# Kernel tuning notes

Hardware: AMD Instinct MI355X
Metric: run time of the kernel (lower is better)

The kernel has to match this reference:

```python
import jax, jax.numpy as jnp
import numpy as np

H = 16  # headNum
D = 1024  # d_model
DK = D // H


def setup_inputs() -> dict:
    key = jax.random.key(0)
    ks = jax.random.split(key, 11)
    B, S = 2, 2048
    scale = 1.0 / np.sqrt(D)
    inp = {
        'query': jax.random.normal(ks[0], (B, S, D), jnp.float32),
        'key':   jax.random.normal(ks[1], (B, S, D), jnp.float32),
        'value': jax.random.normal(ks[2], (B, S, D), jnp.float32),
        # nn.Linear params: W is [out, in], y = x @ W.T + b
        'Wq': jax.random.normal(ks[3], (D, D), jnp.float32) * scale,
        'bq': jnp.zeros((D,), jnp.float32),
        'Wk': jax.random.normal(ks[4], (D, D), jnp.float32) * scale,
        'bk': jnp.zeros((D,), jnp.float32),
        'Wv': jax.random.normal(ks[5], (D, D), jnp.float32) * scale,
        'bv': jnp.zeros((D,), jnp.float32),
        'Wo': jax.random.normal(ks[6], (D, D), jnp.float32) * scale,
        'bo': jnp.zeros((D,), jnp.float32),
    }
    return inp


def reference(query, key, value, Wq, bq, Wk, bk, Wv, bv, Wo, bo):
    B, S, _ = query.shape
    # projections (torch Linear: x @ W.T + b), split heads -> [B, H, S, DK]
    q = (query @ Wq.T + bq).reshape(B, S, H, DK).transpose(0, 2, 1, 3)
    k = (key   @ Wk.T + bk).reshape(B, S, H, DK).transpose(0, 2, 1, 3)
    v = (value @ Wv.T + bv).reshape(B, S, H, DK).transpose(0, 2, 1, 3)
    # scores [B, H, S, S] = Q K^T / sqrt(d_k)  (fully materialized, as in source)
    scores = jnp.einsum('bhqd,bhkd->bhqk', q, k) * (DK ** -0.5)
    p_attn = jax.nn.softmax(scores, axis=-1)  # dropout = identity (eval)
    x = jnp.einsum('bhqk,bhkd->bhqd', p_attn, v)
    x = x.transpose(0, 2, 1, 3).reshape(B, S, H * DK)
    return x @ Wo.T + bo
```

## Files before the change

### kernel.cpp

```cpp
#include <hip/hip_runtime.h>

#define BATCH 2
#define SEQ   2048
#define NH    16
#define DK    64
#define DM    1024
#define MROWS 4096
#define NX    4194304
#define NW    1048576

typedef __attribute__((ext_vector_type(8))) short bf16x8;
typedef __attribute__((ext_vector_type(4))) short bf16x4;
typedef __attribute__((ext_vector_type(4))) float f32x4;
typedef __attribute__((ext_vector_type(4))) unsigned short us16x4;
typedef __attribute__((ext_vector_type(2))) unsigned int u32x2;

#if __has_builtin(__builtin_amdgcn_mfma_f32_16x16x16bf16_1k)
#define MFMA16(a, b, c) __builtin_amdgcn_mfma_f32_16x16x16bf16_1k(a, b, c, 0, 0, 0)
#else
#define MFMA16(a, b, c) (c)
#endif

__device__ __forceinline__ unsigned short f2bf(float f) {
  unsigned int u = __builtin_bit_cast(unsigned int, f);
  u += 0x7FFFu + ((u >> 16) & 1u);
  return (unsigned short)(u >> 16);
}

__device__ __forceinline__ unsigned int pkbf(float hi, float lo) {
#if __has_builtin(__builtin_amdgcn_perm)
  return __builtin_amdgcn_perm(__builtin_bit_cast(unsigned int, hi),
                               __builtin_bit_cast(unsigned int, lo), 0x07060302u);
#else
  return (__builtin_bit_cast(unsigned int, hi) & 0xffff0000u) |
         (__builtin_bit_cast(unsigned int, lo) >> 16);
#endif
}

__device__ __forceinline__ void g2l16(void* lds, const void* g) {
  __builtin_amdgcn_global_load_lds(
      (const __attribute__((address_space(1))) void*)g,
      (__attribute__((address_space(3))) void*)lds, 16, 0, 0);
}

__global__ __launch_bounds__(256) void cast_all(
    const float* __restrict__ q, const float* __restrict__ k, const float* __restrict__ v,
    const float* __restrict__ wq, const float* __restrict__ wk,
    const float* __restrict__ wv, const float* __restrict__ wo,
    unsigned short* __restrict__ dst) {
  size_t e = ((size_t)blockIdx.x * 256 + threadIdx.x) * 4;
  const float* src;
  if      (e < (size_t)NX)        src = q  + e;
  else if (e < (size_t)2*NX)      src = k  + (e - (size_t)NX);
  else if (e < (size_t)3*NX)      src = v  + (e - (size_t)2*NX);
  else if (e < (size_t)3*NX+NW)   src = wq + (e - (size_t)3*NX);
  else if (e < (size_t)3*NX+2*NW) src = wk + (e - (size_t)3*NX-NW);
  else if (e < (size_t)3*NX+3*NW) src = wv + (e - (size_t)3*NX-2*NW);
  else                            src = wo + (e - (size_t)3*NX-3*NW);
  float4 f = *(const float4*)src;
  us16x4 o;
  o[0] = f2bf(f.x); o[1] = f2bf(f.y); o[2] = f2bf(f.z); o[3] = f2bf(f.w);
  *(us16x4*)(dst + e) = o;
}

template <int MODE, int BM>
__global__ __launch_bounds__(256) void gemm_bt(
    const unsigned short* __restrict__ Xbase, const unsigned short* __restrict__ Wbase,
    const float* __restrict__ b0, const float* __restrict__ b1, const float* __restrict__ b2,
    unsigned short* __restrict__ qkv_dst, float* __restrict__ fout, float qscale) {
  constexpr int IM = BM / 32;
  constexpr int ASHOTS = (BM * 32) / 2048;
  const int tid  = threadIdx.x;
  const int lane = tid & 63;
  const int w    = tid >> 6;
  const int wm   = w >> 1, wn = w & 1;
  const int x15  = lane & 15, quad = lane >> 4;
  const int row0 = blockIdx.x * BM;
  const int col0 = blockIdx.y * 128;
  const int z    = blockIdx.z;

  const unsigned short* A  = Xbase + (size_t)z * NX;
  const unsigned short* Wp = Wbase + (size_t)z * NW;
  const float* bias = (MODE == 0) ? (z == 0 ? b0 : (z == 1 ? b1 : b2)) : b0;
  const float zs = (MODE == 0 && z == 0) ? qscale : 1.0f;

  __shared__ __align__(16) unsigned short At[2][BM * 32];
  __shared__ __align__(16) unsigned short Bt[2][128 * 32];

  f32x4 acc[IM][4] = {};

  auto stage = [&](int buf, int kt) {
#pragma unroll
    for (int j = 0; j < ASHOTS; ++j) {
      int e = (j * 256 + tid) * 8;
      int r = e >> 5, c = e & 31;
      g2l16(&At[buf][e], A + (size_t)(row0 + r) * DM + kt + c);
    }
#pragma unroll
    for (int j = 0; j < 2; ++j) {
      int e = (j * 256 + tid) * 8;
      int r = e >> 5, c = e & 31;
      g2l16(&Bt[buf][e], Wp + (size_t)(col0 + r) * DM + kt + c);
    }
  };

  stage(0, 0);
  for (int it = 0; it < DM / 32; ++it) {
    const int cur = it & 1;
    __syncthreads();
    if (it + 1 < DM / 32) stage(cur ^ 1, (it + 1) * 32);
    bf16x8 af[IM], bfv[4];
#pragma unroll
    for (int i = 0; i < IM; ++i)
      af[i] = *(const bf16x8*)&At[cur][(wm * (BM / 2) + i * 16 + x15) * 32 + quad * 8];
#pragma unroll
    for (int jn = 0; jn < 4; ++jn)
      bfv[jn] = *(const bf16x8*)&Bt[cur][(wn * 64 + jn * 16 + x15) * 32 + quad * 8];
#pragma unroll
    for (int i = 0; i < IM; ++i)
#pragma unroll
      for (int jn = 0; jn < 4; ++jn)
        acc[i][jn] = __builtin_amdgcn_mfma_f32_16x16x32_bf16(af[i], bfv[jn], acc[i][jn], 0, 0, 0);
  }

#pragma unroll
  for (int jn = 0; jn < 4; ++jn) {
    const int n = col0 + wn * 64 + jn * 16 + x15;
    const float bv = bias[n];
#pragma unroll
    for (int i = 0; i < IM; ++i) {
      const int m0 = row0 + wm * (BM / 2) + i * 16 + quad * 4;
      if (MODE == 0 && z == 2) {
        us16x4 pk;
#pragma unroll
        for (int r = 0; r < 4; ++r) pk[r] = f2bf(acc[i][jn][r] + bv);
        const int b = m0 >> 11, s = m0 & 2047;
        const int h = n >> 6,  dk = n & 63;
        *(us16x4*)&qkv_dst[(size_t)2 * NX + (((size_t)(b * NH + h) * DK + dk) << 11) + s] = pk;
      } else {
#pragma unroll
        for (int r = 0; r < 4; ++r) {
          const int m = m0 + r;
          float val = (acc[i][jn][r] + bv) * zs;
          if (MODE == 0) {
            const int b = m >> 11, s = m & 2047;
            const int h = n >> 6,  dk = n & 63;
            qkv_dst[(size_t)z * NX + (((size_t)(b * NH + h) * SEQ + s) << 6) + dk] = f2bf(val);
          } else {
            fout[(size_t)m * DM + n] = val;
          }
        }
      }
    }
  }
}

__global__ __launch_bounds__(256, 2) void attn(
    const unsigned short* __restrict__ Qb, const unsigned short* __restrict__ Kb,
    const unsigned short* __restrict__ VTb, unsigned short* __restrict__ AO) {
  const int tid  = threadIdx.x;
  const int lane = tid & 63;
  const int w    = tid >> 6;
  const int x15  = lane & 15, quad = lane >> 4;
  const int lin = (int)(blockIdx.x | (blockIdx.y << 4) | (blockIdx.z << 8));
  const int swz = ((lin & 7) << 6) | (lin >> 3);
  const int qt = swz & 15;
  const int h  = (swz >> 4) & 15;
  const int b  = swz >> 8;
  const size_t bh = ((size_t)(b * NH + h)) * SEQ * DK;
  const unsigned short* Q  = Qb  + bh;
  const unsigned short* K  = Kb  + bh;
  const unsigned short* VT = VTb + bh;
  const int q0 = qt * 128 + w * 32;

  __shared__ __align__(16) unsigned short Kl[2][64 * 64];
  __shared__ __align__(16) unsigned short Vl[2][64 * 64];

  bf16x8 qf[2][2];
#pragma unroll
  for (int qg = 0; qg < 2; ++qg)
#pragma unroll
    for (int ks = 0; ks < 2; ++ks)
      qf[qg][ks] = *(const bf16x8*)&Q[(size_t)(q0 + qg * 16 + x15) * DK + ks * 32 + quad * 8];

  f32x4 po[2][4] = {};
  f32x4 pol[2] = {};
  const bf16x4 vone = {(short)0x3F80, (short)0x3F80, (short)0x3F80, (short)0x3F80};

  const int sK0 = tid >> 3,          sK1 = (tid + 256) >> 3;
  const int dgK0 = (tid & 7) ^ (sK0 & 7), dgK1 = (tid & 7) ^ (sK1 & 7);

  auto stageKV = [&](int buf, int s0) {
    g2l16(&Kl[buf][(size_t)tid * 8],         K + (size_t)(s0 + sK0) * DK + dgK0 * 8);
    g2l16(&Kl[buf][(size_t)(tid + 256) * 8], K + (size_t)(s0 + sK1) * DK + dgK1 * 8);
    g2l16(&Vl[buf][(size_t)tid * 8],         VT + (size_t)sK0 * SEQ + s0 + dgK0 * 8);
    g2l16(&Vl[buf][(size_t)(tid + 256) * 8], VT + (size_t)sK1 * SEQ + s0 + dgK1 * 8);
  };

  stageKV(0, 0);
  for (int s0 = 0; s0 < SEQ; s0 += 64) {
    const int cur = (s0 >> 6) & 1;
    __syncthreads();
    if (s0 + 64 < SEQ) stageKV(cur ^ 1, s0 + 64);

    bf16x8 kf[4][2];
#pragma unroll
    for (int sh = 0; sh < 4; ++sh) {
      const int kbase = (sh * 16 + x15) * 8;
      kf[sh][0] = *(const bf16x8*)&Kl[cur][(kbase + ((0 + quad) ^ (x15 & 7))) * 8];
      kf[sh][1] = *(const bf16x8*)&Kl[cur][(kbase + ((4 + quad) ^ (x15 & 7))) * 8];
    }
    bf16x4 vf[4][4];
#pragma unroll
    for (int sh = 0; sh < 4; ++sh)
#pragma unroll
      for (int nt = 0; nt < 4; ++nt) {
        const int d = nt * 16 + x15;
        const int sg = (sh * 2 + (quad >> 1)) ^ (d & 7);
        vf[sh][nt] = *(const bf16x4*)&Vl[cur][(d * 8 + sg) * 8 + (quad & 1) * 4];
      }

#pragma unroll
    for (int sh = 0; sh < 4; ++sh) {
      bf16x4 pf[2];
#pragma unroll
      for (int qg = 0; qg < 2; ++qg) {
        f32x4 sacc = {};
        sacc = __builtin_amdgcn_mfma_f32_16x16x32_bf16(kf[sh][0], qf[qg][0], sacc, 0, 0, 0);
        sacc = __builtin_amdgcn_mfma_f32_16x16x32_bf16(kf[sh][1], qf[qg][1], sacc, 0, 0, 0);
        float p0 = __builtin_amdgcn_exp2f(sacc[0]);
        float p1 = __builtin_amdgcn_exp2f(sacc[1]);
        float p2 = __builtin_amdgcn_exp2f(sacc[2]);
        float p3 = __builtin_amdgcn_exp2f(sacc[3]);
        u32x2 uu;
        uu[0] = pkbf(p1, p0);
        uu[1] = pkbf(p3, p2);
        pf[qg] = __builtin_bit_cast(bf16x4, uu);
        pol[qg] = MFMA16(vone, pf[qg], pol[qg]);
      }

#pragma unroll
      for (int nt = 0; nt < 4; ++nt) {
        po[0][nt] = MFMA16(vf[sh][nt], pf[0], po[0][nt]);
        po[1][nt] = MFMA16(vf[sh][nt], pf[1], po[1][nt]);
      }
    }
  }

#pragma unroll
  for (int qg = 0; qg < 2; ++qg) {
    const float inv = 1.0f / pol[qg][0];
    const int s = q0 + qg * 16 + x15;
#pragma unroll
    for (int nt = 0; nt < 4; ++nt) {
      us16x4 pk;
#pragma unroll
      for (int r = 0; r < 4; ++r) pk[r] = f2bf(po[qg][nt][r] * inv);
      const int d = nt * 16 + quad * 4;
      *(us16x4*)&AO[((size_t)(b * SEQ + s)) * DM + h * DK + d] = pk;
    }
  }
}

extern "C" void kernel_launch(void* const* d_in, const int* in_sizes, int n_in,
                              void* d_out, int out_size, void* d_ws, size_t ws_size,
                              hipStream_t stream) {
  const float* q  = (const float*)d_in[0];
  const float* k  = (const float*)d_in[1];
  const float* v  = (const float*)d_in[2];
  const float* wq = (const float*)d_in[3];
  const float* bq = (const float*)d_in[4];
  const float* wk = (const float*)d_in[5];
  const float* bk = (const float*)d_in[6];
  const float* wv = (const float*)d_in[7];
  const float* bv = (const float*)d_in[8];
  const float* wo = (const float*)d_in[9];
  const float* bo = (const float*)d_in[10];
  float* out = (float*)d_out;

  unsigned short* ws = (unsigned short*)d_ws;
  unsigned short* Xq = ws;
  unsigned short* Wb = ws + (size_t)3 * NX;
  unsigned short* Qb = ws + (size_t)3 * NX + 4 * NW;
  unsigned short* AO = Qb + (size_t)3 * NX;

  const float qscale = 0.125f * 1.4426950408889634f;

  cast_all<<<16384, 256, 0, stream>>>(q, k, v, wq, wk, wv, wo, ws);
  gemm_bt<0, 128><<<dim3(32, 8, 3), 256, 0, stream>>>(Xq, Wb, bq, bk, bv, Qb, nullptr, qscale);
  attn<<<dim3(16, 16, 2), 256, 0, stream>>>(Qb, Qb + (size_t)NX, Qb + (size_t)2 * NX, AO);
  gemm_bt<1, 64><<<dim3(64, 8, 1), 256, 0, stream>>>(AO, Wb + (size_t)3 * NW, bo, bo, bo,
                                                     nullptr, out, 1.0f);
}
```

Before: 223.9 us.

## Split attention KV tile across wave pairs and reduce partial outputs via LDS

Each block's four waves are regrouped into two query halves (64 rows each) by two key halves, so every wave loads only half of the K/V fragments from LDS per tile and holds 64 query rows. Row sums are now kept in VALU adds instead of an extra MFMA against a ones vector, and the final output is formed by reducing the two key-split partial accumulators through shared memory, which reuses the K/V staging buffers. The change also raises wave priority around the MFMA section. It trades fewer LDS reads and MFMAs per tile for more accumulator registers and an epilogue reduction with extra barriers.

Measured after the change: 220.0 us. Within noise of the previous version (-1.7%).

```diff
diff --git a/kernel.cpp b/kernel.cpp
--- a/kernel.cpp
+++ b/kernel.cpp
@@ -161,6 +161,8 @@
   const int tid  = threadIdx.x;
   const int lane = tid & 63;
   const int w    = tid >> 6;
+  const int wq   = w & 1;
+  const int ws   = w >> 1;
   const int x15  = lane & 15, quad = lane >> 4;
   const int lin = (int)(blockIdx.x | (blockIdx.y << 4) | (blockIdx.z << 8));
   const int swz = ((lin & 7) << 6) | (lin >> 3);
@@ -171,30 +173,32 @@
   const unsigned short* Q  = Qb  + bh;
   const unsigned short* K  = Kb  + bh;
   const unsigned short* VT = VTb + bh;
-  const int q0 = qt * 128 + w * 32;
-
-  __shared__ __align__(16) unsigned short Kl[2][64 * 64];
-  __shared__ __align__(16) unsigned short Vl[2][64 * 64];
-
-  bf16x8 qf[2][2];
-#pragma unroll
-  for (int qg = 0; qg < 2; ++qg)
+  const int q0 = qt * 128;
+
+  __shared__ __align__(16) unsigned char smem[2 * 64 * 68 * 4];
+  unsigned short* Kl = (unsigned short*)smem;
+  unsigned short* Vl = (unsigned short*)(smem + 16384);
+  float* Ored = (float*)smem;
+  __shared__ float lbuf[2][4][128];
+
+  bf16x8 qf[4][2];
+#pragma unroll
+  for (int qgi = 0; qgi < 4; ++qgi)
 #pragma unroll
     for (int ks = 0; ks < 2; ++ks)
-      qf[qg][ks] = *(const bf16x8*)&Q[(size_t)(q0 + qg * 16 + x15) * DK + ks * 32 + quad * 8];
-
-  f32x4 po[2][4] = {};
-  f32x4 pol[2] = {};
-  const bf16x4 vone = {(short)0x3F80, (short)0x3F80, (short)0x3F80, (short)0x3F80};
+      qf[qgi][ks] = *(const bf16x8*)&Q[(size_t)(q0 + wq * 64 + qgi * 16 + x15) * DK + ks * 32 + quad * 8];
+
+  f32x4 po[4][4] = {};
+  float pol[4] = {0.f, 0.f, 0.f, 0.f};
 
   const int sK0 = tid >> 3,          sK1 = (tid + 256) >> 3;
   const int dgK0 = (tid & 7) ^ (sK0 & 7), dgK1 = (tid & 7) ^ (sK1 & 7);
 
   auto stageKV = [&](int buf, int s0) {
-    g2l16(&Kl[buf][(size_t)tid * 8],         K + (size_t)(s0 + sK0) * DK + dgK0 * 8);
-    g2l16(&Kl[buf][(size_t)(tid + 256) * 8], K + (size_t)(s0 + sK1) * DK + dgK1 * 8);
-    g2l16(&Vl[buf][(size_t)tid * 8],         VT + (size_t)sK0 * SEQ + s0 + dgK0 * 8);
-    g2l16(&Vl[buf][(size_t)(tid + 256) * 8], VT + (size_t)sK1 * SEQ + s0 + dgK1 * 8);
+    g2l16(&Kl[buf * 4096 + tid * 8],         K + (size_t)(s0 + sK0) * DK + dgK0 * 8);
+    g2l16(&Kl[buf * 4096 + (tid + 256) * 8], K + (size_t)(s0 + sK1) * DK + dgK1 * 8);
+    g2l16(&Vl[buf * 4096 + tid * 8],         VT + (size_t)sK0 * SEQ + s0 + dgK0 * 8);
+    g2l16(&Vl[buf * 4096 + (tid + 256) * 8], VT + (size_t)sK1 * SEQ + s0 + dgK1 * 8);
   };
 
   stageKV(0, 0);
@@ -203,62 +207,84 @@
     __syncthreads();
     if (s0 + 64 < SEQ) stageKV(cur ^ 1, s0 + 64);
 
-    bf16x8 kf[4][2];
-#pragma unroll
-    for (int sh = 0; sh < 4; ++sh) {
+    bf16x8 kf[2][2];
+#pragma unroll
+    for (int shi = 0; shi < 2; ++shi) {
+      const int sh = ws * 2 + shi;
       const int kbase = (sh * 16 + x15) * 8;
-      kf[sh][0] = *(const bf16x8*)&Kl[cur][(kbase + ((0 + quad) ^ (x15 & 7))) * 8];
-      kf[sh][1] = *(const bf16x8*)&Kl[cur][(kbase + ((4 + quad) ^ (x15 & 7))) * 8];
-    }
-    bf16x4 vf[4][4];
-#pragma unroll
-    for (int sh = 0; sh < 4; ++sh)
+      kf[shi][0] = *(const bf16x8*)&Kl[cur * 4096 + (kbase + ((0 + quad) ^ (x15 & 7))) * 8];
+      kf[shi][1] = *(const bf16x8*)&Kl[cur * 4096 + (kbase + ((4 + quad) ^ (x15 & 7))) * 8];
+    }
+    bf16x4 vf[2][4];
+#pragma unroll
+    for (int shi = 0; shi < 2; ++shi)
 #pragma unroll
       for (int nt = 0; nt < 4; ++nt) {
         const int d = nt * 16 + x15;
-        const int sg = (sh * 2 + (quad >> 1)) ^ (d & 7);
-        vf[sh][nt] = *(const bf16x4*)&Vl[cur][(d * 8 + sg) * 8 + (quad & 1) * 4];
+        const int sg = ((ws * 2 + shi) * 2 + (quad >> 1)) ^ (d & 7);
+        vf[shi][nt] = *(const bf16x4*)&Vl[cur * 4096 + (d * 8 + sg) * 8 + (quad & 1) * 4];
       }
 
-#pragma unroll
-    for (int sh = 0; sh < 4; ++sh) {
-      bf16x4 pf[2];
-#pragma unroll
-      for (int qg = 0; qg < 2; ++qg) {
+    __builtin_amdgcn_s_setprio(1);
+#pragma unroll
+    for (int shi = 0; shi < 2; ++shi) {
+#pragma unroll
+      for (int qgi = 0; qgi < 4; ++qgi) {
         f32x4 sacc = {};
-        sacc = __builtin_amdgcn_mfma_f32_16x16x32_bf16(kf[sh][0], qf[qg][0], sacc, 0, 0, 0);
-        sacc = __builtin_amdgcn_mfma_f32_16x16x32_bf16(kf[sh][1], qf[qg][1], sacc, 0, 0, 0);
+        sacc = __builtin_amdgcn_mfma_f32_16x16x32_bf16(kf[shi][0], qf[qgi][0], sacc, 0, 0, 0);
+        sacc = __builtin_amdgcn_mfma_f32_16x16x32_bf16(kf[shi][1], qf[qgi][1], sacc, 0, 0, 0);
         float p0 = __builtin_amdgcn_exp2f(sacc[0]);
         float p1 = __builtin_amdgcn_exp2f(sacc[1]);
         float p2 = __builtin_amdgcn_exp2f(sacc[2]);
         float p3 = __builtin_amdgcn_exp2f(sacc[3]);
+        pol[qgi] += (p0 + p1) + (p2 + p3);
         u32x2 uu;
         uu[0] = pkbf(p1, p0);
         uu[1] = pkbf(p3, p2);
-        pf[qg] = __builtin_bit_cast(bf16x4, uu);
-        pol[qg] = MFMA16(vone, pf[qg], pol[qg]);
+        bf16x4 pf = __builtin_bit_cast(bf16x4, uu);
+#pragma unroll
+        for (int nt = 0; nt < 4; ++nt)
+          po[qgi][nt] = MFMA16(vf[shi][nt], pf, po[qgi][nt]);
       }
-
-#pragma unroll
-      for (int nt = 0; nt < 4; ++nt) {
-        po[0][nt] = MFMA16(vf[sh][nt], pf[0], po[0][nt]);
-        po[1][nt] = MFMA16(vf[sh][nt], pf[1], po[1][nt]);
-      }
-    }
+    }
+    __builtin_amdgcn_s_setprio(0);
   }
 
 #pragma unroll
-  for (int qg = 0; qg < 2; ++qg) {
-    const float inv = 1.0f / pol[qg][0];
-    const int s = q0 + qg * 16 + x15;
-#pragma unroll
-    for (int nt = 0; nt < 4; ++nt) {
+  for (int qgi = 0; qgi < 4; ++qgi)
+    lbuf[ws][quad][wq * 64 + qgi * 16 + x15] = pol[qgi];
+  __syncthreads();
+
+  const int qq = tid >> 2;
+  const int d0 = (tid & 3) * 16;
+#pragma unroll
+  for (int rw = 0; rw < 2; ++rw) {
+    if (wq == rw) {
+#pragma unroll
+      for (int qgi = 0; qgi < 4; ++qgi)
+#pragma unroll
+        for (int nt = 0; nt < 4; ++nt)
+          *(f32x4*)&Ored[(ws * 64 + qgi * 16 + x15) * 68 + nt * 16 + quad * 4] = po[qgi][nt];
+    }
+    __syncthreads();
+    float ls = 0.f;
+#pragma unroll
+    for (int w2 = 0; w2 < 2; ++w2)
+#pragma unroll
+      for (int qd = 0; qd < 4; ++qd)
+        ls += lbuf[w2][qd][rw * 64 + qq];
+    const float inv = 1.0f / ls;
+    const size_t orow = ((size_t)(b * SEQ + q0 + rw * 64 + qq)) * DM + h * DK + d0;
+#pragma unroll
+    for (int c = 0; c < 4; ++c) {
+      f32x4 sa = *(const f32x4*)&Ored[(0 * 64 + qq) * 68 + d0 + c * 4];
+      f32x4 sb = *(const f32x4*)&Ored[(1 * 64 + qq) * 68 + d0 + c * 4];
       us16x4 pk;
 #pragma unroll
-      for (int r = 0; r < 4; ++r) pk[r] = f2bf(po[qg][nt][r] * inv);
-      const int d = nt * 16 + quad * 4;
-      *(us16x4*)&AO[((size_t)(b * SEQ + s)) * DM + h * DK + d] = pk;
-    }
+      for (int r = 0; r < 4; ++r) pk[r] = f2bf((sa[r] + sb[r]) * inv);
+      *(us16x4*)&AO[orow + c * 4] = pk;
+    }
+    __syncthreads();
   }
 }
 
```
